# Optimization experiments

Hardware: AMD Instinct MI355X
Metric: run time of the kernel (lower is better)

The kernel has to match this reference:

```python
import jax, jax.numpy as jnp
import numpy as np

B, D, NNZ = 64, 8192, 1024      # batch, data_dim, nonzeros per row (exact)
DE, DQK = 256, 256              # id_embed_dim, qk_dim


def setup_inputs() -> dict:
    key = jax.random.key(0)
    k_pos, k_val, k_e, k_wq, k_bq, k_wk, k_bk = jax.random.split(key, 7)
    # x: [B, D] with exactly NNZ nonzero entries per row
    pos = jax.random.uniform(k_pos, (B, D)).argsort(axis=1)[:, :NNZ]  # [B, NNZ]
    vals = jax.random.normal(k_val, (B, NNZ), dtype=jnp.float32)
    vals = jnp.where(vals == 0.0, 1.0, vals)
    x = jnp.zeros((B, D), jnp.float32).at[jnp.arange(B)[:, None], pos].set(vals)
    # parameters (Embedding(D+1, DE), Linear(DE->DQK) x2)
    E = jax.random.normal(k_e, (D + 1, DE), dtype=jnp.float32)
    lim = 1.0 / np.sqrt(DE)
    Wq = jax.random.uniform(k_wq, (DQK, DE), minval=-lim, maxval=lim, dtype=jnp.float32)
    bq = jax.random.uniform(k_bq, (DQK,), minval=-lim, maxval=lim, dtype=jnp.float32)
    Wk = jax.random.uniform(k_wk, (DQK, DE), minval=-lim, maxval=lim, dtype=jnp.float32)
    bk = jax.random.uniform(k_bk, (DQK,), minval=-lim, maxval=lim, dtype=jnp.float32)
    return {"t": 0, "x": x, "E": E, "Wq": Wq, "bq": bq, "Wk": Wk, "bk": bk}


def _condense(x):
    # Vectorized equivalent of the per-row nonzero gather; rows have exactly
    # NNZ nonzeros so max_len == NNZ and positions stay in ascending order
    # (matching torch.nonzero) via a stable sort on the zero-mask.
    mask = (x != 0.0)
    idx = jnp.argsort(jnp.where(mask, 0, 1), axis=1, stable=True)[:, :NNZ]  # [B, NNZ]
    v = jnp.take_along_axis(x, idx, axis=1)                                 # [B, NNZ]
    p = idx + 1                                                             # 1-based ids
    return v, p, idx


def reference(t, x, E, Wq, bq, Wk, bk):
    v, p, idx = _condense(x)                    # [B,L], [B,L]
    e = E[p]                                    # [B,L,DE] embedding gather
    q = jnp.einsum('bld,od->blo', e, Wq) + bq   # [B,L,DQK]
    k = jnp.einsum('bld,od->blo', e, Wk) + bk
    scale = 1.0 / jnp.sqrt(jnp.asarray(DQK, x.dtype))
    S = jnp.einsum('bid,bjd->bij', q, k) * scale  # [B,L,L]
    fx = jnp.einsum('bij,bi->bj', S, v)           # [B,L]
    v_new = v + v * fx
    # decondense: scatter back to dense [B, D]
    y = jnp.zeros_like(x).at[jnp.arange(B)[:, None], idx].set(v_new)
    return y
```

## Files before the change

### kernel.cpp

```cpp
#include <hip/hip_runtime.h>
#include <hip/hip_bf16.h>

constexpr int B   = 64;
constexpr int D   = 8192;
constexpr int DE  = 256;
constexpr int DQK = 256;
constexpr float SCALE = 0.0625f;

constexpr int NKC = 64;
constexpr int KD  = D / NKC;

constexpr size_t OFF_MT    = 0;
constexpr size_t OFF_AUX   = 65536;
constexpr size_t OFF_WPART = 66112;
constexpr size_t OFF_Z     = 1114688;
constexpr size_t OFF_C     = 1131072;

__global__ __launch_bounds__(256, 2) void kA(
    const float* __restrict__ x, const float* __restrict__ E,
    const float* __restrict__ Wq, const float* __restrict__ bq,
    const float* __restrict__ Wk, const float* __restrict__ bk,
    float* __restrict__ ws)
{
    __shared__ __align__(16) char smem[68608];
    const int blk = blockIdx.x;
    const int tid = threadIdx.x;

    if (blk < 256) {
        const int kc  = blk >> 2;
        const int tqb = blk & 3;
        float (*Xl)[132] = (float(*)[132])smem;
        float (*Et)[68]  = (float(*)[68])(smem + 33792);

        #pragma unroll
        for (int i = 0; i < 8; ++i) {
            int f4 = i * 256 + tid;
            int r = f4 >> 5, c4 = f4 & 31;
            float4 v = *reinterpret_cast<const float4*>(
                x + (size_t)r * D + kc * KD + 4 * c4);
            *reinterpret_cast<float4*>(&Xl[r][4 * c4]) = v;
        }
        #pragma unroll
        for (int i = 0; i < 8; ++i) {
            int f4 = i * 256 + tid;
            int r = f4 >> 4, c4 = f4 & 15;
            float4 v = *reinterpret_cast<const float4*>(
                E + (size_t)(kc * KD + r + 1) * DE + tqb * 64 + 4 * c4);
            *reinterpret_cast<float4*>(&Et[r][4 * c4]) = v;
        }
        __syncthreads();

        const int bq4 = tid >> 4;
        const int tq4 = tid & 15;
        float acc[4][4] = {};
        #pragma unroll 4
        for (int k = 0; k < KD; ++k) {
            const float e0 = Et[k][4 * tq4 + 0];
            const float e1 = Et[k][4 * tq4 + 1];
            const float e2 = Et[k][4 * tq4 + 2];
            const float e3 = Et[k][4 * tq4 + 3];
            #pragma unroll
            for (int i = 0; i < 4; ++i) {
                const float xv = Xl[4 * bq4 + i][k];
                acc[i][0] += xv * e0; acc[i][1] += xv * e1;
                acc[i][2] += xv * e2; acc[i][3] += xv * e3;
            }
        }
        float* WP = ws + OFF_WPART + (size_t)kc * (64 * 256);
        #pragma unroll
        for (int i = 0; i < 4; ++i)
            *reinterpret_cast<float4*>(
                WP + (size_t)(4 * bq4 + i) * 256 + tqb * 64 + 4 * tq4) =
                make_float4(acc[i][0], acc[i][1], acc[i][2], acc[i][3]);
    } else if (blk < 320) {
        const int mb = blk - 256;
        float (*Aq)[33] = (float(*)[33])smem;
        float (*Bk)[33] = (float(*)[33])(smem + 4224);
        const int bi = mb >> 3, bj = mb & 7;
        const int I0 = bi * 32, J0 = bj * 32;
        const int lr = tid >> 5;
        const int lc = tid & 31;
        float acc[4] = {0.f, 0.f, 0.f, 0.f};
        for (int oc = 0; oc < DQK; oc += 32) {
            #pragma unroll
            for (int r = 0; r < 4; ++r) {
                int oo = lr + 8 * r;
                Aq[oo][lc] = Wq[(size_t)(oc + oo) * DE + I0 + lc];
                Bk[oo][lc] = Wk[(size_t)(oc + oo) * DE + J0 + lc];
            }
            __syncthreads();
            #pragma unroll
            for (int oo = 0; oo < 32; ++oo) {
                float bv = Bk[oo][lc];
                #pragma unroll
                for (int r = 0; r < 4; ++r)
                    acc[r] += Aq[oo][lr + 8 * r] * bv;
            }
            __syncthreads();
        }
        float* MT = ws + OFF_MT;
        #pragma unroll
        for (int r = 0; r < 4; ++r)
            MT[(size_t)(I0 + lr + 8 * r) * DE + (J0 + lc)] = acc[r] * SCALE;
    } else {
        float* sb0 = (float*)smem;
        float* sb1 = sb0 + 256;
        float* rp  = sb1 + 256;
        float* aux = ws + OFF_AUX;
        sb0[tid] = bq[tid];
        sb1[tid] = bk[tid];
        __syncthreads();
        float a0 = 0.f, a1 = 0.f;
        #pragma unroll 8
        for (int o = 0; o < DQK; ++o) {
            a0 += Wk[(size_t)o * DE + tid] * sb0[o];
            a1 += Wq[(size_t)o * DE + tid] * sb1[o];
        }
        aux[tid]       = a0 * SCALE;
        aux[256 + tid] = a1 * SCALE;
        rp[tid] = sb0[tid] * sb1[tid];
        __syncthreads();
        if (tid < 128) rp[tid] += rp[tid + 128];
        __syncthreads();
        if (tid < 64) {
            float v = rp[tid] + rp[tid + 64];
            for (int off = 32; off; off >>= 1) v += __shfl_xor(v, off);
            if (tid == 0) aux[512] = v * SCALE;
        }
    }
}

__global__ __launch_bounds__(256) void kB(
    const float* __restrict__ x, float* __restrict__ ws)
{
    const int b   = blockIdx.x;
    const int tid = threadIdx.x;
    __shared__ float wl[256];
    __shared__ float red[256];
    __shared__ float s_s;

    float ps = 0.f;
    const float4* xr = reinterpret_cast<const float4*>(x + (size_t)b * D);
    #pragma unroll 8
    for (int i = tid; i < D / 4; i += 256) {
        float4 v = xr[i];
        ps += (v.x + v.y) + (v.z + v.w);
    }
    red[tid] = ps;

    float w = 0.f;
    #pragma unroll 8
    for (int kc = 0; kc < NKC; ++kc)
        w += ws[OFF_WPART + (size_t)kc * (64 * 256) + (size_t)b * 256 + tid];
    wl[tid] = w;
    __syncthreads();

    if (tid < 128) red[tid] += red[tid + 128];
    __syncthreads();
    if (tid < 64) {
        float v = red[tid] + red[tid + 64];
        for (int off = 32; off; off >>= 1) v += __shfl_xor(v, off);
        if (tid == 0) s_s = v;
    }
    __syncthreads();
    const float sv = s_s;

    float z = sv * ws[OFF_AUX + tid];
    #pragma unroll 8
    for (int d2 = 0; d2 < 256; ++d2)
        z += wl[d2] * ws[OFF_MT + (size_t)d2 * 256 + tid];
    ws[OFF_Z + (size_t)tid * B + b] = z;

    red[tid] = ws[OFF_AUX + 256 + tid] * w;
    __syncthreads();
    if (tid < 128) red[tid] += red[tid + 128];
    __syncthreads();
    if (tid < 64) {
        float v = red[tid] + red[tid + 64];
        for (int off = 32; off; off >>= 1) v += __shfl_xor(v, off);
        if (tid == 0) ws[OFF_C + b] = v + sv * ws[OFF_AUX + 512];
    }
}

__global__ __launch_bounds__(256, 2) void kC(
    const float* __restrict__ x, const float* __restrict__ E,
    const float* __restrict__ ws, float* __restrict__ y)
{
    const int d0  = blockIdx.x * 32;
    const int tid = threadIdx.x;

    __shared__ float Zl[256][64];
    __shared__ float Et[32][68];

    #pragma unroll
    for (int i = 0; i < 64; ++i)
        (&Zl[0][0])[i * 256 + tid] = ws[OFF_Z + (size_t)i * 256 + tid];
    __syncthreads();

    const int dq  = tid >> 4;
    const int bq4 = tid & 15;
    float acc[2][4] = {};

    for (int ks = 0; ks < 4; ++ks) {
        #pragma unroll
        for (int i = 0; i < 2; ++i) {
            int f4 = i * 256 + tid;
            int r = f4 >> 4, c4 = f4 & 15;
            float4 v = *reinterpret_cast<const float4*>(
                E + (size_t)(d0 + r + 1) * DE + ks * 64 + 4 * c4);
            *reinterpret_cast<float4*>(&Et[r][4 * c4]) = v;
        }
        __syncthreads();
        #pragma unroll 4
        for (int tt = 0; tt < 64; ++tt) {
            const float4 z4 = *reinterpret_cast<const float4*>(
                &Zl[ks * 64 + tt][4 * bq4]);
            const float e0 = Et[2 * dq + 0][tt];
            const float e1 = Et[2 * dq + 1][tt];
            acc[0][0] += e0 * z4.x; acc[0][1] += e0 * z4.y;
            acc[0][2] += e0 * z4.z; acc[0][3] += e0 * z4.w;
            acc[1][0] += e1 * z4.x; acc[1][1] += e1 * z4.y;
            acc[1][2] += e1 * z4.z; acc[1][3] += e1 * z4.w;
        }
        __syncthreads();
    }

    #pragma unroll
    for (int i = 0; i < 2; ++i)
        *reinterpret_cast<float4*>(&Et[2 * dq + i][4 * bq4]) =
            make_float4(acc[i][0], acc[i][1], acc[i][2], acc[i][3]);
    __syncthreads();

    {
        const int b  = tid >> 2;
        const int ds = (tid & 3) * 8;
        const float cc = ws[OFF_C + b];
        const float* xr = x + (size_t)b * D + d0 + ds;
        float*       yr = y + (size_t)b * D + d0 + ds;
        #pragma unroll
        for (int k4 = 0; k4 < 2; ++k4) {
            float4 xv = *reinterpret_cast<const float4*>(xr + 4 * k4);
            float4 yv;
            yv.x = xv.x * (1.f + Et[ds + 4 * k4 + 0][b] + cc);
            yv.y = xv.y * (1.f + Et[ds + 4 * k4 + 1][b] + cc);
            yv.z = xv.z * (1.f + Et[ds + 4 * k4 + 2][b] + cc);
            yv.w = xv.w * (1.f + Et[ds + 4 * k4 + 3][b] + cc);
            *reinterpret_cast<float4*>(yr + 4 * k4) = yv;
        }
    }
}

extern "C" void kernel_launch(void* const* d_in, const int* in_sizes, int n_in,
                              void* d_out, int out_size, void* d_ws, size_t ws_size,
                              hipStream_t stream) {
    const float* x  = (const float*)d_in[1];
    const float* E  = (const float*)d_in[2];
    const float* Wq = (const float*)d_in[3];
    const float* bq = (const float*)d_in[4];
    const float* Wk = (const float*)d_in[5];
    const float* bk = (const float*)d_in[6];
    float* y  = (float*)d_out;
    float* ws = (float*)d_ws;

    hipLaunchKernelGGL(kA, dim3(321), dim3(256), 0, stream, x, E, Wq, bq, Wk, bk, ws);
    hipLaunchKernelGGL(kB, dim3(B),   dim3(256), 0, stream, x, ws);
    hipLaunchKernelGGL(kC, dim3(256), dim3(256), 0, stream, x, E, ws, y);
}
```

Before: 115.6 us.

## Vectorize LDS reads in GEMM loops and split kB across output quarters

The inner loops of kA and kC now read shared memory as float4 over four k-steps instead of scalar loads, which cuts LDS instruction count. kB is relaunched with 256 blocks (four per batch row), each computing a quarter of the z outputs with a split-K reduction in shared memory, so the small 64-block kernel gets more parallelism. kC's Z staging uses float4 loads. In exchange, each kB block redundantly recomputes the row sum and the w partial-sum reduction, and the c term is computed only by the tq==0 blocks.

```diff
diff --git a/kernel.cpp b/kernel.cpp
--- a/kernel.cpp
+++ b/kernel.cpp
@@ -53,17 +53,27 @@
         const int bq4 = tid >> 4;
         const int tq4 = tid & 15;
         float acc[4][4] = {};
-        #pragma unroll 4
-        for (int k = 0; k < KD; ++k) {
-            const float e0 = Et[k][4 * tq4 + 0];
-            const float e1 = Et[k][4 * tq4 + 1];
-            const float e2 = Et[k][4 * tq4 + 2];
-            const float e3 = Et[k][4 * tq4 + 3];
-            #pragma unroll
-            for (int i = 0; i < 4; ++i) {
-                const float xv = Xl[4 * bq4 + i][k];
-                acc[i][0] += xv * e0; acc[i][1] += xv * e1;
-                acc[i][2] += xv * e2; acc[i][3] += xv * e3;
+        #pragma unroll 2
+        for (int k0 = 0; k0 < KD; k0 += 4) {
+            float4 xv[4], ev[4];
+            #pragma unroll
+            for (int i = 0; i < 4; ++i)
+                xv[i] = *reinterpret_cast<const float4*>(&Xl[4 * bq4 + i][k0]);
+            #pragma unroll
+            for (int kk = 0; kk < 4; ++kk)
+                ev[kk] = *reinterpret_cast<const float4*>(&Et[k0 + kk][4 * tq4]);
+            #pragma unroll
+            for (int kk = 0; kk < 4; ++kk) {
+                const float e0 = ((const float*)&ev[kk])[0];
+                const float e1 = ((const float*)&ev[kk])[1];
+                const float e2 = ((const float*)&ev[kk])[2];
+                const float e3 = ((const float*)&ev[kk])[3];
+                #pragma unroll
+                for (int i = 0; i < 4; ++i) {
+                    const float xvk = ((const float*)&xv[i])[kk];
+                    acc[i][0] += xvk * e0; acc[i][1] += xvk * e1;
+                    acc[i][2] += xvk * e2; acc[i][3] += xvk * e3;
+                }
             }
         }
         float* WP = ws + OFF_WPART + (size_t)kc * (64 * 256);
@@ -133,11 +143,18 @@
 __global__ __launch_bounds__(256) void kB(
     const float* __restrict__ x, float* __restrict__ ws)
 {
-    const int b   = blockIdx.x;
+    const int blk = blockIdx.x;
+    const int b = blk >> 2, tq = blk & 3;
     const int tid = threadIdx.x;
     __shared__ float wl[256];
     __shared__ float red[256];
     __shared__ float s_s;
+
+    float w = 0.f;
+    #pragma unroll 8
+    for (int kc = 0; kc < NKC; ++kc)
+        w += ws[OFF_WPART + (size_t)kc * (64 * 256) + (size_t)b * 256 + tid];
+    wl[tid] = w;
 
     float ps = 0.f;
     const float4* xr = reinterpret_cast<const float4*>(x + (size_t)b * D);
@@ -147,14 +164,7 @@
         ps += (v.x + v.y) + (v.z + v.w);
     }
     red[tid] = ps;
-
-    float w = 0.f;
-    #pragma unroll 8
-    for (int kc = 0; kc < NKC; ++kc)
-        w += ws[OFF_WPART + (size_t)kc * (64 * 256) + (size_t)b * 256 + tid];
-    wl[tid] = w;
-    __syncthreads();
-
+    __syncthreads();
     if (tid < 128) red[tid] += red[tid + 128];
     __syncthreads();
     if (tid < 64) {
@@ -165,20 +175,34 @@
     __syncthreads();
     const float sv = s_s;
 
-    float z = sv * ws[OFF_AUX + tid];
+    const int tl = tid & 63, dq = tid >> 6;
+    const int t = tq * 64 + tl;
+    float zp = 0.f;
     #pragma unroll 8
-    for (int d2 = 0; d2 < 256; ++d2)
-        z += wl[d2] * ws[OFF_MT + (size_t)d2 * 256 + tid];
-    ws[OFF_Z + (size_t)tid * B + b] = z;
-
-    red[tid] = ws[OFF_AUX + 256 + tid] * w;
-    __syncthreads();
-    if (tid < 128) red[tid] += red[tid + 128];
+    for (int i = 0; i < 64; ++i) {
+        const int d2 = dq * 64 + i;
+        zp += wl[d2] * ws[OFF_MT + (size_t)d2 * 256 + t];
+    }
+    __syncthreads();
+    red[tid] = zp;
     __syncthreads();
     if (tid < 64) {
-        float v = red[tid] + red[tid + 64];
-        for (int off = 32; off; off >>= 1) v += __shfl_xor(v, off);
-        if (tid == 0) ws[OFF_C + b] = v + sv * ws[OFF_AUX + 512];
+        float z = red[tid] + red[tid + 64] + red[tid + 128] + red[tid + 192]
+                + sv * ws[OFF_AUX + tq * 64 + tid];
+        ws[OFF_Z + (size_t)(tq * 64 + tid) * B + b] = z;
+    }
+
+    if (tq == 0) {
+        __syncthreads();
+        red[tid] = ws[OFF_AUX + 256 + tid] * wl[tid];
+        __syncthreads();
+        if (tid < 128) red[tid] += red[tid + 128];
+        __syncthreads();
+        if (tid < 64) {
+            float v = red[tid] + red[tid + 64];
+            for (int off = 32; off; off >>= 1) v += __shfl_xor(v, off);
+            if (tid == 0) ws[OFF_C + b] = v + sv * ws[OFF_AUX + 512];
+        }
     }
 }
 
@@ -193,8 +217,11 @@
     __shared__ float Et[32][68];
 
     #pragma unroll
-    for (int i = 0; i < 64; ++i)
-        (&Zl[0][0])[i * 256 + tid] = ws[OFF_Z + (size_t)i * 256 + tid];
+    for (int i = 0; i < 16; ++i) {
+        int f4 = i * 256 + tid;
+        float4 v = *reinterpret_cast<const float4*>(ws + OFF_Z + 4 * (size_t)f4);
+        *reinterpret_cast<float4*>(&Zl[0][0] + 4 * f4) = v;
+    }
     __syncthreads();
 
     const int dq  = tid >> 4;
@@ -211,16 +238,24 @@
             *reinterpret_cast<float4*>(&Et[r][4 * c4]) = v;
         }
         __syncthreads();
-        #pragma unroll 4
-        for (int tt = 0; tt < 64; ++tt) {
-            const float4 z4 = *reinterpret_cast<const float4*>(
-                &Zl[ks * 64 + tt][4 * bq4]);
-            const float e0 = Et[2 * dq + 0][tt];
-            const float e1 = Et[2 * dq + 1][tt];
-            acc[0][0] += e0 * z4.x; acc[0][1] += e0 * z4.y;
-            acc[0][2] += e0 * z4.z; acc[0][3] += e0 * z4.w;
-            acc[1][0] += e1 * z4.x; acc[1][1] += e1 * z4.y;
-            acc[1][2] += e1 * z4.z; acc[1][3] += e1 * z4.w;
+        #pragma unroll 2
+        for (int t0 = 0; t0 < 64; t0 += 4) {
+            float4 zv[4];
+            #pragma unroll
+            for (int kk = 0; kk < 4; ++kk)
+                zv[kk] = *reinterpret_cast<const float4*>(
+                    &Zl[ks * 64 + t0 + kk][4 * bq4]);
+            const float4 e0v = *reinterpret_cast<const float4*>(&Et[2 * dq + 0][t0]);
+            const float4 e1v = *reinterpret_cast<const float4*>(&Et[2 * dq + 1][t0]);
+            #pragma unroll
+            for (int kk = 0; kk < 4; ++kk) {
+                const float e0 = ((const float*)&e0v)[kk];
+                const float e1 = ((const float*)&e1v)[kk];
+                acc[0][0] += e0 * zv[kk].x; acc[0][1] += e0 * zv[kk].y;
+                acc[0][2] += e0 * zv[kk].z; acc[0][3] += e0 * zv[kk].w;
+                acc[1][0] += e1 * zv[kk].x; acc[1][1] += e1 * zv[kk].y;
+                acc[1][2] += e1 * zv[kk].z; acc[1][3] += e1 * zv[kk].w;
+            }
         }
         __syncthreads();
     }
@@ -263,6 +298,6 @@
     float* ws = (float*)d_ws;
 
     hipLaunchKernelGGL(kA, dim3(321), dim3(256), 0, stream, x, E, Wq, bq, Wk, bk, ws);
-    hipLaunchKernelGGL(kB, dim3(B),   dim3(256), 0, stream, x, ws);
+    hipLaunchKernelGGL(kB, dim3(256), dim3(256), 0, stream, x, ws);
     hipLaunchKernelGGL(kC, dim3(256), dim3(256), 0, stream, x, E, ws, y);
 }
```

New measurement: 109.8 us. 5.0% less time.
